# Performance work log

Hardware: AMD Instinct MI355X
Metric: run time of the kernel (lower is better)

Reference implementation:

```python
import jax, jax.numpy as jnp
import numpy as np

G = 512          # number of graphs
N = 512          # nodes per graph (equal-sized graphs)
NN = G * N       # total nodes
EG = 8192        # edges per graph (avg degree 16)
C_IN, HID, OUT, K = 128, 32, 2, 20
LATENT = HID * 2 + 1  # 65 = conv1 kernel size & stride


def _gcn(x, W, b, src, dst, deg_inv_sqrt):
    """GCNConv with self-loops: out = D^-1/2 (A+I) D^-1/2 (x W) + b."""
    h = x @ W                                        # [NN, out]
    norm = deg_inv_sqrt[src] * deg_inv_sqrt[dst]     # [E]
    agg = jnp.zeros_like(h).at[dst].add(h[src] * norm[:, None])
    # self-loop message: norm_ii = deg_inv_sqrt[i]^2
    agg = agg + h * (deg_inv_sqrt * deg_inv_sqrt)[:, None]
    return agg + b


def setup_inputs() -> dict:
    key = jax.random.key(0)
    ks = jax.random.split(key, 24)
    x = jax.random.normal(ks[0], (NN, C_IN), jnp.float32)
    offs = (jnp.arange(G, dtype=jnp.int32) * N)[:, None]
    src = (jax.random.randint(ks[1], (G, EG), 0, N, jnp.int32) + offs).reshape(-1)
    dst = (jax.random.randint(ks[2], (G, EG), 0, N, jnp.int32) + offs).reshape(-1)
    edge_index = jnp.stack([src, dst])               # [2, G*EG]
    batch = jnp.repeat(jnp.arange(G, dtype=jnp.int32), N)

    def lin(k, fan_in, shape):
        return jax.random.normal(k, shape, jnp.float32) / np.sqrt(fan_in)

    return {
        "x": x, "edge_index": edge_index, "batch": batch,
        "W0": lin(ks[3], C_IN, (C_IN, HID)), "b0": jnp.zeros((HID,), jnp.float32),
        "W1": lin(ks[4], HID, (HID, HID)),   "b1": jnp.zeros((HID,), jnp.float32),
        "W2": lin(ks[5], HID, (HID, 1)),     "b2": jnp.zeros((1,), jnp.float32),
        "conv1_w": lin(ks[6], LATENT, (16, 1, LATENT)), "conv1_b": jnp.zeros((16,), jnp.float32),
        "conv2_w": lin(ks[7], 16 * 5, (32, 16, 5)),     "conv2_b": jnp.zeros((32,), jnp.float32),
        "lin1_w": lin(ks[8], 192, (192, 128)), "lin1_b": jnp.zeros((128,), jnp.float32),
        "lin2_w": lin(ks[9], 128, (128, OUT)), "lin2_b": jnp.zeros((OUT,), jnp.float32),
    }


def reference(x, edge_index, batch, W0, b0, W1, b1, W2, b2,
              conv1_w, conv1_b, conv2_w, conv2_b,
              lin1_w, lin1_b, lin2_w, lin2_b):
    src, dst = edge_index[0], edge_index[1]
    deg = jnp.zeros((NN,), jnp.float32).at[dst].add(1.0) + 1.0  # +1 self-loop
    dis = jax.lax.rsqrt(deg)

    x1 = jnp.tanh(_gcn(x,  W0, b0, src, dst, dis))   # [NN, 32]
    x2 = jnp.tanh(_gcn(x1, W1, b1, src, dst, dis))   # [NN, 32]
    x3 = jnp.tanh(_gcn(x2, W2, b2, src, dst, dis))   # [NN, 1]
    feat = jnp.concatenate([x1, x2, x3], axis=-1)    # [NN, 65]

    # global_sort_pool: equal-sized contiguous graphs -> reshape, sort by last
    # channel (descending) within each graph, take top-k nodes.
    fg = feat.reshape(G, N, LATENT)
    idx = jnp.argsort(-fg[..., -1], axis=1)[:, :K]                 # [G, K]
    pooled = jnp.take_along_axis(fg, idx[:, :, None], axis=1)      # [G, K, 65]

    # conv1: Conv1d(1,16,kernel=65,stride=65) over flattened [G,1,K*65]
    # == per-sorted-node matmul with the 65-wide kernel.
    h = jax.nn.relu(jnp.einsum('gkc,oc->gok', pooled, conv1_w[:, 0, :])
                    + conv1_b[None, :, None])                      # [G, 16, K]
    h = h.reshape(G, 16, K // 2, 2).max(-1)                        # MaxPool1d(2,2) -> [G,16,10]
    h = jax.nn.relu(
        jax.lax.conv_general_dilated(h, conv2_w, (1,), 'VALID',
                                     dimension_numbers=('NCH', 'OIH', 'NCH'))
        + conv2_b[None, :, None])                                  # [G, 32, 6]
    h = h.reshape(G, -1)                                           # [G, 192]
    h = jax.nn.relu(h @ lin1_w + lin1_b)
    # dropout is identity in eval mode
    return h @ lin2_w + lin2_b                                     # [G, 2]
```

## Files before the change

### kernel.cpp

```cpp
#include <hip/hip_runtime.h>
#include <math.h>

#define G_ 512
#define N_ 512
#define NN_ (G_*N_)
#define EG_ 8192
#define EGP 8704
#define CIN_ 128
#define HID_ 32
#define K_ 20
#define LAT_ 65
#define NSTRIPE 4
#define SW 8
#define HP 513

#define EPS_REL 1.8e-7f

__global__ __launch_bounds__(512) void csr2_kernel(const int* __restrict__ src,
                                                   const int* __restrict__ dst,
                                                   unsigned short* __restrict__ srcl,
                                                   int* __restrict__ gstart,
                                                   unsigned short* __restrict__ nperm,
                                                   double* __restrict__ disd) {
    __shared__ int cnt[N_];
    __shared__ int startv[N_];
    __shared__ int tmpv[N_];
    __shared__ int cursor[N_];
    __shared__ int hcur[128];
    __shared__ unsigned short binE[EGP];
    int g = blockIdx.x, tid = threadIdx.x;
    const int* ds = dst + (size_t)g * EG_;
    const int* ss = src + (size_t)g * EG_;
    int nb = g * N_;

    cnt[tid] = 0;
    if (tid < 128) hcur[tid] = 0;
    for (int i = tid; i < EGP; i += 512) binE[i] = 0xFFFF;
    __syncthreads();
    for (int e = tid; e < EG_; e += 512) atomicAdd(&cnt[ds[e] - nb], 1);
    __syncthreads();

    int mydeg = cnt[tid];
    int db = mydeg < 127 ? mydeg : 127;
    atomicAdd(&hcur[db], 1);
    __syncthreads();
    if (tid == 0) {
        int run = 0;
        for (int d = 0; d < 128; ++d) { int v = hcur[d]; hcur[d] = run; run += v; }
    }
    __syncthreads();
    {
        int slot = atomicAdd(&hcur[db], 1);
        nperm[g * N_ + slot] = (unsigned short)tid;
    }

    int pc = (mydeg + 1) & ~1;
    startv[tid] = pc;
    __syncthreads();
    for (int off = 1; off < N_; off <<= 1) {
        tmpv[tid] = startv[tid] + (tid >= off ? startv[tid - off] : 0);
        __syncthreads();
        startv[tid] = tmpv[tid];
        __syncthreads();
    }

    int excl = startv[tid] - pc;
    cursor[tid] = excl;
    gstart[g * (N_ + 1) + tid] = excl;
    if (tid == 511) gstart[g * (N_ + 1) + N_] = startv[511];
    disd[nb + tid] = 1.0 / sqrt((double)(mydeg + 1));
    __syncthreads();

    for (int e = tid; e < EG_; e += 512) {
        int d = ds[e] - nb;
        int slot = atomicAdd(&cursor[d], 1);
        binE[slot] = (unsigned short)e;
    }
    __syncthreads();

    {
        int n = mydeg;
        for (int i = 1; i < n; ++i) {
            unsigned short key = binE[excl + i];
            int j = i - 1;
            while (j >= 0 && binE[excl + j] > key) {
                binE[excl + j + 1] = binE[excl + j];
                --j;
            }
            binE[excl + j + 1] = key;
        }
    }
    __syncthreads();

    for (int i = tid; i < EGP; i += 512) {
        unsigned short e = binE[i];
        srcl[(size_t)g * EGP + i] =
            (e == 0xFFFF) ? (unsigned short)N_ : (unsigned short)(ss[e] - nb);
    }
}

template <int CI>
__global__ __launch_bounds__(256) void mm_kernel(const float* __restrict__ xin,
                                                 const float* __restrict__ W,
                                                 double* __restrict__ h) {
    __shared__ float sx[64][CI + 4];
    __shared__ float sWt[HID_][CI + 5];
    int tid = threadIdx.x;
    for (int i = tid; i < CI * HID_; i += 256) {
        int c = i / HID_, o = i % HID_;
        sWt[o][c] = W[i];
    }
    size_t base = (size_t)blockIdx.x * 64;
    const float4* xsrc = (const float4*)(xin + base * CI);
    for (int i = tid; i < 64 * CI / 4; i += 256) {
        int row = i / (CI / 4), col = (i % (CI / 4)) * 4;
        *(float4*)&sx[row][col] = xsrc[i];
    }
    __syncthreads();

    int o2 = tid & 15, q = tid >> 4;
    int n0 = q * 4;
    double acc[4][2];
#pragma unroll
    for (int j = 0; j < 4; ++j) { acc[j][0] = 0.0; acc[j][1] = 0.0; }

    for (int c = 0; c < CI; c += 4) {
        float4 wa = *(const float4*)&sWt[2 * o2][c];
        float4 wb = *(const float4*)&sWt[2 * o2 + 1][c];
        double w0a = (double)wa.x, w1a = (double)wa.y,
               w2a = (double)wa.z, w3a = (double)wa.w;
        double w0b = (double)wb.x, w1b = (double)wb.y,
               w2b = (double)wb.z, w3b = (double)wb.w;
#pragma unroll
        for (int j = 0; j < 4; ++j) {
            float4 v = *(const float4*)&sx[n0 + j][c];
            double vx = (double)v.x, vy = (double)v.y,
                   vz = (double)v.z, vw = (double)v.w;
            acc[j][0] = fma(vx, w0a, acc[j][0]);
            acc[j][0] = fma(vy, w1a, acc[j][0]);
            acc[j][0] = fma(vz, w2a, acc[j][0]);
            acc[j][0] = fma(vw, w3a, acc[j][0]);
            acc[j][1] = fma(vx, w0b, acc[j][1]);
            acc[j][1] = fma(vy, w1b, acc[j][1]);
            acc[j][1] = fma(vz, w2b, acc[j][1]);
            acc[j][1] = fma(vw, w3b, acc[j][1]);
        }
    }
    int stripe = o2 >> 2;
    int oc = (o2 & 3) * 2;
#pragma unroll
    for (int j = 0; j < 4; ++j) {
        double2 val;
        val.x = acc[j][0];
        val.y = acc[j][1];
        *(double2*)&h[(((size_t)stripe) * NN_ + base + n0 + j) * SW + oc] = val;
    }
}

__global__ __launch_bounds__(512) void agg_kernel(const double* __restrict__ h,
                                                  const unsigned short* __restrict__ srcl,
                                                  const int* __restrict__ gstart,
                                                  const unsigned short* __restrict__ nperm,
                                                  const double* __restrict__ disd,
                                                  const float* __restrict__ bias,
                                                  float* __restrict__ xoutf) {
    __shared__ double hd2[SW * HP];
    __shared__ unsigned short ssrc[EGP];
    __shared__ unsigned short sstart[N_ + 2];
    __shared__ unsigned short sperm[N_];
    int g = blockIdx.x, st = blockIdx.y, tid = threadIdx.x;
    size_t nbase = (size_t)g * N_;

    for (int i = tid; i < EGP; i += 512) ssrc[i] = srcl[(size_t)g * EGP + i];
    for (int i = tid; i <= N_; i += 512) sstart[i] = (unsigned short)gstart[g * (N_ + 1) + i];
    sperm[tid] = nperm[g * N_ + tid];
    __syncthreads();

    const double* hraw = h + ((size_t)st * NN_ + nbase) * SW;
    const double* dg = disd + nbase;
    for (int i = tid; i < N_ * SW; i += 512) {
        int s = i >> 3, oc = i & 7;
        hd2[oc * HP + s] = hraw[i] * dg[s];
    }
    if (tid < SW) hd2[tid * HP + N_] = -0.0;
    __syncthreads();

    int oc = tid & 7, grp = tid >> 3;
    const double* hrow = hd2 + oc * HP;
    const unsigned int* ssrc32 = (const unsigned int*)ssrc;
    double b = (double)bias[st * SW + oc];

    int nn[8], e0h[8], e1h[8];
    double a[8];
    int mx = 0;
#pragma unroll
    for (int j = 0; j < 8; ++j) {
        int n = sperm[grp * 8 + j];
        nn[j] = n;
        e0h[j] = sstart[n] >> 1;
        e1h[j] = sstart[n + 1] >> 1;
        a[j] = 0.0;
        int d = e1h[j] - e0h[j];
        mx = d > mx ? d : mx;
    }
    for (int t = 0; t < mx; ++t) {
#pragma unroll
        for (int j = 0; j < 8; ++j) {
            int idx = e0h[j] + t;
            if (idx < e1h[j]) {
                unsigned int pr = ssrc32[idx];
                a[j] += hrow[pr & 0xFFFFu];
                a[j] += hrow[pr >> 16];
            }
        }
    }
#pragma unroll
    for (int j = 0; j < 8; ++j) {
        int n = nn[j];
        double dn = dg[n];
        double v = a[j] * dn + hrow[n] * dn + b;
        xoutf[(nbase + n) * HID_ + st * SW + oc] = tanhf((float)v);
    }
}

__global__ __launch_bounds__(512) void gcn3_head_kernel(
        const float* __restrict__ xin,
        const float* __restrict__ W2,
        const float* __restrict__ b2,
        const unsigned short* __restrict__ srcl,
        const int* __restrict__ gstart,
        const double* __restrict__ disd,
        const float* __restrict__ x1,
        const float* __restrict__ x2,
        const float* __restrict__ c1w, const float* __restrict__ c1b,
        const float* __restrict__ c2w, const float* __restrict__ c2b,
        const float* __restrict__ l1w, const float* __restrict__ l1b,
        const float* __restrict__ l2w, const float* __restrict__ l2b,
        float* __restrict__ out) {
    __shared__ double h1[N_ + 1];
    __shared__ unsigned short ssrc[EGP];
    __shared__ int sstart[N_ + 1];
    __shared__ double sdis[N_ + 1];
    __shared__ float sv[N_];
    __shared__ int   topk[K_];
    __shared__ float pooled[K_][LAT_];
    __shared__ float c1[16][K_];
    __shared__ float mp[16][10];
    __shared__ float c2s[32 * 6];
    __shared__ float l1s[128];
    int g = blockIdx.x, tid = threadIdx.x;
    size_t nbase = (size_t)g * N_;

    for (int i = tid; i < EGP; i += 512) ssrc[i] = srcl[(size_t)g * EGP + i];
    for (int i = tid; i <= N_; i += 512) sstart[i] = gstart[g * (N_ + 1) + i];
    if (tid == 0) { h1[N_] = -0.0; sdis[N_] = 1.0; }
    if (tid < K_) topk[tid] = tid;
    int n = tid;
    {
        double a = 0.0;
#pragma unroll
        for (int c = 0; c < HID_; ++c)
            a = fma((double)xin[(nbase + n) * HID_ + c], (double)W2[c], a);
        h1[n] = a;
        sdis[n] = disd[nbase + n];
    }
    __syncthreads();

    {
        int e0 = sstart[n], e1 = sstart[n + 1];
        double a = 0.0;
        for (int e = e0; e < e1; ++e) {
            int s = ssrc[e];
            a += h1[s] * sdis[s];
        }
        double dn = sdis[n];
        double v = a * dn + h1[n] * dn * dn + (double)b2[0];
        sv[n] = (float)tanh(v);
    }
    __syncthreads();

    {
        float v = sv[n];
        int rank = 0;
        for (int j = 0; j < N_; ++j) {
            float u = sv[j];
            float mag = fmaxf(fabsf(u), fabsf(v));
            bool tie = fabsf(u - v) <= EPS_REL * mag;
            bool beats = tie ? (j < n) : (u > v);
            rank += beats;
        }
        if (rank < K_) topk[rank] = n;
    }
    __syncthreads();

    for (int i = tid; i < K_ * LAT_; i += 512) {
        int k = i / LAT_, c = i % LAT_;
        int node = topk[k];
        float f;
        if (c < HID_)            f = x1[(nbase + node) * HID_ + c];
        else if (c < 2 * HID_)   f = x2[(nbase + node) * HID_ + (c - HID_)];
        else                     f = sv[node];
        pooled[k][c] = f;
    }
    __syncthreads();

    for (int i = tid; i < 16 * K_; i += 512) {
        int o = i / K_, k = i % K_;
        float acc = c1b[o];
        for (int c = 0; c < LAT_; ++c) acc += pooled[k][c] * c1w[o * LAT_ + c];
        c1[o][k] = fmaxf(acc, 0.f);
    }
    __syncthreads();

    for (int i = tid; i < 160; i += 512) {
        int o = i / 10, t = i % 10;
        mp[o][t] = fmaxf(c1[o][2 * t], c1[o][2 * t + 1]);
    }
    __syncthreads();

    for (int i = tid; i < 192; i += 512) {
        int o = i / 6, t = i % 6;
        float acc = c2b[o];
        for (int ic = 0; ic < 16; ++ic)
#pragma unroll
            for (int j = 0; j < 5; ++j)
                acc += mp[ic][t + j] * c2w[(o * 16 + ic) * 5 + j];
        c2s[o * 6 + t] = fmaxf(acc, 0.f);
    }
    __syncthreads();

    for (int i = tid; i < 128; i += 512) {
        float acc = l1b[i];
        for (int c = 0; c < 192; ++c) acc += c2s[c] * l1w[c * 128 + i];
        l1s[i] = fmaxf(acc, 0.f);
    }
    __syncthreads();

    for (int i = tid; i < 2; i += 512) {
        float acc = l2b[i];
        for (int c = 0; c < 128; ++c) acc += l1s[c] * l2w[c * 2 + i];
        out[g * 2 + i] = acc;
    }
}

extern "C" void kernel_launch(void* const* d_in, const int* in_sizes, int n_in,
                              void* d_out, int out_size, void* d_ws, size_t ws_size,
                              hipStream_t stream) {
    const float* x   = (const float*)d_in[0];
    const int*   ei  = (const int*)d_in[1];
    const float* W0  = (const float*)d_in[3];
    const float* b0  = (const float*)d_in[4];
    const float* W1  = (const float*)d_in[5];
    const float* b1  = (const float*)d_in[6];
    const float* W2  = (const float*)d_in[7];
    const float* b2  = (const float*)d_in[8];
    const float* c1w = (const float*)d_in[9];
    const float* c1b = (const float*)d_in[10];
    const float* c2w = (const float*)d_in[11];
    const float* c2b = (const float*)d_in[12];
    const float* l1w = (const float*)d_in[13];
    const float* l1b = (const float*)d_in[14];
    const float* l2w = (const float*)d_in[15];
    const float* l2b = (const float*)d_in[16];

    const int* src = ei;
    const int* dst = ei + (size_t)G_ * EG_;

    char* wsb = (char*)d_ws;
    double* h64  = (double*)wsb;                 wsb += (size_t)NN_ * HID_ * 8;
    unsigned short* srcl = (unsigned short*)wsb; wsb += (size_t)G_ * EGP * 2;
    int* gstart = (int*)wsb;                     wsb += (size_t)G_ * (N_ + 1) * 4;
    unsigned short* nperm = (unsigned short*)wsb; wsb += (size_t)G_ * N_ * 2;
    double* disd = (double*)wsb;                 wsb += (size_t)NN_ * 8;
    float*  x1f  = (float*)wsb;                  wsb += (size_t)NN_ * HID_ * 4;
    float*  x2f  = (float*)wsb;                  wsb += (size_t)NN_ * HID_ * 4;

    dim3 agrid(G_, NSTRIPE);
    csr2_kernel<<<G_, 512, 0, stream>>>(src, dst, srcl, gstart, nperm, disd);
    mm_kernel<CIN_><<<NN_ / 64, 256, 0, stream>>>(x, W0, h64);
    agg_kernel<<<agrid, 512, 0, stream>>>(h64, srcl, gstart, nperm, disd, b0, x1f);
    mm_kernel<HID_><<<NN_ / 64, 256, 0, stream>>>(x1f, W1, h64);
    agg_kernel<<<agrid, 512, 0, stream>>>(h64, srcl, gstart, nperm, disd, b1, x2f);
    gcn3_head_kernel<<<G_, 512, 0, stream>>>(x2f, W2, b2, srcl, gstart, disd,
                                             x1f, x2f, c1w, c1b, c2w, c2b,
                                             l1w, l1b, l2w, l2b, (float*)d_out);
}
```

Measured before the change: 344.4 us.

## Fuse dense transform into per-graph aggregation kernel, dropping h64 intermediate

Merges the GCN linear transform into the aggregation kernel: each (stripe, graph) block computes x·W for its 8 output channels per node directly into shared memory, then aggregates. This removes the double-precision h intermediate buffer round trip and two kernel launches. In exchange, each graph's input rows are reread by all four stripe blocks, and per-thread row loads are strided rather than coalesced. The grid is reordered so stripe blocks of a graph run adjacently for L2 reuse.

```diff
diff --git a/kernel.cpp b/kernel.cpp
--- a/kernel.cpp
+++ b/kernel.cpp
@@ -100,87 +100,58 @@
 }
 
 template <int CI>
-__global__ __launch_bounds__(256) void mm_kernel(const float* __restrict__ xin,
-                                                 const float* __restrict__ W,
-                                                 double* __restrict__ h) {
-    __shared__ float sx[64][CI + 4];
-    __shared__ float sWt[HID_][CI + 5];
-    int tid = threadIdx.x;
-    for (int i = tid; i < CI * HID_; i += 256) {
-        int c = i / HID_, o = i % HID_;
-        sWt[o][c] = W[i];
-    }
-    size_t base = (size_t)blockIdx.x * 64;
-    const float4* xsrc = (const float4*)(xin + base * CI);
-    for (int i = tid; i < 64 * CI / 4; i += 256) {
-        int row = i / (CI / 4), col = (i % (CI / 4)) * 4;
-        *(float4*)&sx[row][col] = xsrc[i];
-    }
-    __syncthreads();
-
-    int o2 = tid & 15, q = tid >> 4;
-    int n0 = q * 4;
-    double acc[4][2];
-#pragma unroll
-    for (int j = 0; j < 4; ++j) { acc[j][0] = 0.0; acc[j][1] = 0.0; }
-
-    for (int c = 0; c < CI; c += 4) {
-        float4 wa = *(const float4*)&sWt[2 * o2][c];
-        float4 wb = *(const float4*)&sWt[2 * o2 + 1][c];
-        double w0a = (double)wa.x, w1a = (double)wa.y,
-               w2a = (double)wa.z, w3a = (double)wa.w;
-        double w0b = (double)wb.x, w1b = (double)wb.y,
-               w2b = (double)wb.z, w3b = (double)wb.w;
-#pragma unroll
-        for (int j = 0; j < 4; ++j) {
-            float4 v = *(const float4*)&sx[n0 + j][c];
-            double vx = (double)v.x, vy = (double)v.y,
-                   vz = (double)v.z, vw = (double)v.w;
-            acc[j][0] = fma(vx, w0a, acc[j][0]);
-            acc[j][0] = fma(vy, w1a, acc[j][0]);
-            acc[j][0] = fma(vz, w2a, acc[j][0]);
-            acc[j][0] = fma(vw, w3a, acc[j][0]);
-            acc[j][1] = fma(vx, w0b, acc[j][1]);
-            acc[j][1] = fma(vy, w1b, acc[j][1]);
-            acc[j][1] = fma(vz, w2b, acc[j][1]);
-            acc[j][1] = fma(vw, w3b, acc[j][1]);
-        }
-    }
-    int stripe = o2 >> 2;
-    int oc = (o2 & 3) * 2;
-#pragma unroll
-    for (int j = 0; j < 4; ++j) {
-        double2 val;
-        val.x = acc[j][0];
-        val.y = acc[j][1];
-        *(double2*)&h[(((size_t)stripe) * NN_ + base + n0 + j) * SW + oc] = val;
-    }
-}
-
-__global__ __launch_bounds__(512) void agg_kernel(const double* __restrict__ h,
-                                                  const unsigned short* __restrict__ srcl,
-                                                  const int* __restrict__ gstart,
-                                                  const unsigned short* __restrict__ nperm,
-                                                  const double* __restrict__ disd,
-                                                  const float* __restrict__ bias,
-                                                  float* __restrict__ xoutf) {
+__global__ __launch_bounds__(512) void agg_mm_kernel(
+        const float* __restrict__ xin,
+        const float* __restrict__ W,
+        const unsigned short* __restrict__ srcl,
+        const int* __restrict__ gstart,
+        const unsigned short* __restrict__ nperm,
+        const double* __restrict__ disd,
+        const float* __restrict__ bias,
+        float* __restrict__ xoutf) {
     __shared__ double hd2[SW * HP];
     __shared__ unsigned short ssrc[EGP];
     __shared__ unsigned short sstart[N_ + 2];
-    __shared__ unsigned short sperm[N_];
-    int g = blockIdx.x, st = blockIdx.y, tid = threadIdx.x;
+    __shared__ double sWd[CI * SW];
+    int st = blockIdx.x, g = blockIdx.y, tid = threadIdx.x;
     size_t nbase = (size_t)g * N_;
 
     for (int i = tid; i < EGP; i += 512) ssrc[i] = srcl[(size_t)g * EGP + i];
     for (int i = tid; i <= N_; i += 512) sstart[i] = (unsigned short)gstart[g * (N_ + 1) + i];
-    sperm[tid] = nperm[g * N_ + tid];
-    __syncthreads();
-
-    const double* hraw = h + ((size_t)st * NN_ + nbase) * SW;
+    for (int i = tid; i < CI * SW; i += 512) {
+        int c = i >> 3, oc = i & 7;
+        sWd[i] = (double)W[c * HID_ + st * SW + oc];
+    }
+    __syncthreads();
+
     const double* dg = disd + nbase;
-    for (int i = tid; i < N_ * SW; i += 512) {
-        int s = i >> 3, oc = i & 7;
-        hd2[oc * HP + s] = hraw[i] * dg[s];
+    {
+        int s = tid;
+        const float4* xr4 = (const float4*)(xin + (nbase + s) * CI);
+        double a[SW];
+#pragma unroll
+        for (int oc = 0; oc < SW; ++oc) a[oc] = 0.0;
+#pragma unroll
+        for (int c0 = 0; c0 < CI; c0 += 16) {
+            float4 v0 = xr4[c0 / 4 + 0];
+            float4 v1 = xr4[c0 / 4 + 1];
+            float4 v2 = xr4[c0 / 4 + 2];
+            float4 v3 = xr4[c0 / 4 + 3];
+            float xc[16] = { v0.x, v0.y, v0.z, v0.w, v1.x, v1.y, v1.z, v1.w,
+                             v2.x, v2.y, v2.z, v2.w, v3.x, v3.y, v3.z, v3.w };
+#pragma unroll
+            for (int cc = 0; cc < 16; ++cc) {
+                double xv = (double)xc[cc];
+                const double* wrow = &sWd[(c0 + cc) * SW];
+#pragma unroll
+                for (int oc = 0; oc < SW; ++oc)
+                    a[oc] = fma(xv, wrow[oc], a[oc]);
+            }
+        }
+        double ds = dg[s];
+#pragma unroll
+        for (int oc = 0; oc < SW; ++oc)
+            hd2[oc * HP + s] = a[oc] * ds;
     }
     if (tid < SW) hd2[tid * HP + N_] = -0.0;
     __syncthreads();
@@ -195,7 +166,7 @@
     int mx = 0;
 #pragma unroll
     for (int j = 0; j < 8; ++j) {
-        int n = sperm[grp * 8 + j];
+        int n = nperm[g * N_ + grp * 8 + j];
         nn[j] = n;
         e0h[j] = sstart[n] >> 1;
         e1h[j] = sstart[n + 1] >> 1;
@@ -367,7 +338,6 @@
     const int* dst = ei + (size_t)G_ * EG_;
 
     char* wsb = (char*)d_ws;
-    double* h64  = (double*)wsb;                 wsb += (size_t)NN_ * HID_ * 8;
     unsigned short* srcl = (unsigned short*)wsb; wsb += (size_t)G_ * EGP * 2;
     int* gstart = (int*)wsb;                     wsb += (size_t)G_ * (N_ + 1) * 4;
     unsigned short* nperm = (unsigned short*)wsb; wsb += (size_t)G_ * N_ * 2;
@@ -375,12 +345,10 @@
     float*  x1f  = (float*)wsb;                  wsb += (size_t)NN_ * HID_ * 4;
     float*  x2f  = (float*)wsb;                  wsb += (size_t)NN_ * HID_ * 4;
 
-    dim3 agrid(G_, NSTRIPE);
+    dim3 agrid(NSTRIPE, G_);
     csr2_kernel<<<G_, 512, 0, stream>>>(src, dst, srcl, gstart, nperm, disd);
-    mm_kernel<CIN_><<<NN_ / 64, 256, 0, stream>>>(x, W0, h64);
-    agg_kernel<<<agrid, 512, 0, stream>>>(h64, srcl, gstart, nperm, disd, b0, x1f);
-    mm_kernel<HID_><<<NN_ / 64, 256, 0, stream>>>(x1f, W1, h64);
-    agg_kernel<<<agrid, 512, 0, stream>>>(h64, srcl, gstart, nperm, disd, b1, x2f);
+    agg_mm_kernel<CIN_><<<agrid, 512, 0, stream>>>(x, W0, srcl, gstart, nperm, disd, b0, x1f);
+    agg_mm_kernel<HID_><<<agrid, 512, 0, stream>>>(x1f, W1, srcl, gstart, nperm, disd, b1, x2f);
     gcn3_head_kernel<<<G_, 512, 0, stream>>>(x2f, W2, b2, srcl, gstart, disd,
                                              x1f, x2f, c1w, c1b, c2w, c2b,
                                              l1w, l1b, l2w, l2b, (float*)d_out);
```

New measurement: 342.1 us. About the same (-0.7%).
